# Optimization experiments

Measured on AMD Instinct MI355X. Metric: run time of the kernel, lower is better.

Reference implementation:

```python
import jax, jax.numpy as jnp
import numpy as np

ROUTER_TEMP = 1.0
SCALING = 16.0 / 8.0  # lora_alpha / r


def setup_inputs() -> dict:
    key = jax.random.key(0)
    ks = jax.random.split(key, 6)
    B, S, D, O, E, R = 4, 2048, 4096, 4096, 8, 8
    return {
        "x": jax.random.normal(ks[0], (B, S, D), dtype=jnp.float32),
        "W_base": jax.random.normal(ks[1], (O, D), dtype=jnp.float32) * 0.02,
        "b_base": jax.random.normal(ks[2], (O,), dtype=jnp.float32) * 0.02,
        "lora_A": jax.random.normal(ks[3], (E, R, D), dtype=jnp.float32) * 0.02,
        "lora_B": jax.random.normal(ks[4], (E, O, R), dtype=jnp.float32) * 0.02,
        "router_W": jax.random.normal(ks[5], (E, D), dtype=jnp.float32) * 0.02,
        "router_b": jnp.zeros((E,), dtype=jnp.float32),
    }


def reference(x, W_base, b_base, lora_A, lora_B, router_W, router_b):
    # Base linear: [B,S,D] @ [D,O] + b -> [B,S,O]
    result = jnp.einsum("bsd,od->bso", x, W_base) + b_base

    # Router over mean-pooled sequence: [B,D] -> [B,E]
    x_router = x.mean(axis=1)
    logits = jnp.einsum("bd,ed->be", x_router, router_W) + router_b
    weights = jax.nn.softmax(logits / ROUTER_TEMP, axis=-1)  # [B,E]

    # Per-expert LoRA: down-project to small r, weight by router, up-project.
    h = jnp.einsum("bsd,erd->bser", x, lora_A)            # [B,S,E,r] (small)
    hw = h * weights[:, None, :, None]                      # router-weighted
    lora_out = jnp.einsum("bser,eor->bso", hw, lora_B)     # [B,S,O]

    return result + lora_out * SCALING
```

## Files before the change

kernel.cpp:

```cpp
#include <hip/hip_runtime.h>
#include <hip/hip_bf16.h>


typedef unsigned short u16;
typedef __attribute__((ext_vector_type(8))) short short8;
typedef __attribute__((ext_vector_type(8))) unsigned short u16x8;
typedef __attribute__((ext_vector_type(4))) float f32x4;

#define AS1(p) ((const __attribute__((address_space(1))) void*)(p))
#define AS3(p) ((__attribute__((address_space(3))) void*)(p))

constexpr int KM   = 4224;
constexpr int NOUT = 4096;

__device__ __forceinline__ u16 f2bf(float f) {
    union { float f; unsigned int u; } v; v.f = f;
    unsigned int r = v.u + 0x7fffu + ((v.u >> 16) & 1u);
    return (u16)(r >> 16);
}

__global__ __launch_bounds__(256) void k_convx(const float* __restrict__ x,
                                               u16* __restrict__ Xext,
                                               float* __restrict__ colpart) {
    const int t = threadIdx.x;
    const int row0 = (blockIdx.x >> 7) * 2048 + (blockIdx.x & 127) * 16;
    float4 cs[4] = {{0,0,0,0},{0,0,0,0},{0,0,0,0},{0,0,0,0}};
    for (int r = 0; r < 16; ++r) {
        size_t roff = (size_t)(row0 + r) * 4096;
        #pragma unroll
        for (int g = 0; g < 2; ++g) {
            int col = g * 2048 + t * 8;
            const float4* p = (const float4*)(x + roff + col);
            float4 v0 = p[0], v1 = p[1];
            cs[2*g].x += v0.x; cs[2*g].y += v0.y; cs[2*g].z += v0.z; cs[2*g].w += v0.w;
            cs[2*g+1].x += v1.x; cs[2*g+1].y += v1.y; cs[2*g+1].z += v1.z; cs[2*g+1].w += v1.w;
            u16x8 o;
            o[0]=f2bf(v0.x); o[1]=f2bf(v0.y); o[2]=f2bf(v0.z); o[3]=f2bf(v0.w);
            o[4]=f2bf(v1.x); o[5]=f2bf(v1.y); o[6]=f2bf(v1.z); o[7]=f2bf(v1.w);
            *(u16x8*)(Xext + (size_t)(row0 + r) * KM + col) = o;
        }
    }
    float* cp = colpart + (size_t)blockIdx.x * 4096;
    #pragma unroll
    for (int g = 0; g < 2; ++g) {
        *(float4*)(cp + g * 2048 + t * 8)     = cs[2*g];
        *(float4*)(cp + g * 2048 + t * 8 + 4) = cs[2*g+1];
    }
}

__global__ __launch_bounds__(256) void k_logit(const float* __restrict__ colpart,
                                               const float* __restrict__ rW,
                                               float* __restrict__ logits) {
    const int b = blockIdx.x >> 3, e = blockIdx.x & 7;
    const int t = threadIdx.x;
    const int c0 = t * 16;
    float4 rw[4];
    #pragma unroll
    for (int j = 0; j < 4; ++j) rw[j] = *(const float4*)(rW + e * 4096 + c0 + j * 4);
    float acc = 0.f;
    for (int sc = 0; sc < 128; ++sc) {
        const float4* p = (const float4*)(colpart + ((size_t)(b * 128 + sc)) * 4096 + c0);
        #pragma unroll
        for (int j = 0; j < 4; ++j) {
            float4 v = p[j];
            acc += v.x * rw[j].x + v.y * rw[j].y + v.z * rw[j].z + v.w * rw[j].w;
        }
    }
    __shared__ float red[256];
    red[t] = acc;
    __syncthreads();
    for (int off = 128; off > 0; off >>= 1) {
        if (t < off) red[t] += red[t + off];
        __syncthreads();
    }
    if (t == 0) logits[b * 8 + e] = red[0];
}

__global__ void k_conv8(const float* __restrict__ src, u16* __restrict__ dst) {
    size_t t = (size_t)blockIdx.x * 256 + threadIdx.x;
    size_t base = t * 8;
    size_t row = base >> 12;
    int col = (int)(base & 4095);
    const float4* s = (const float4*)(src + base);
    float4 v0 = s[0], v1 = s[1];
    u16x8 o;
    o[0]=f2bf(v0.x); o[1]=f2bf(v0.y); o[2]=f2bf(v0.z); o[3]=f2bf(v0.w);
    o[4]=f2bf(v1.x); o[5]=f2bf(v1.y); o[6]=f2bf(v1.z); o[7]=f2bf(v1.w);
    *(u16x8*)(dst + row * KM + col) = o;
}

__global__ void k_wlora(const float* __restrict__ lb, u16* __restrict__ Wext) {
    int f = blockIdx.x * 256 + threadIdx.x;
    int e = f >> 15, o = (f >> 3) & 4095, r = f & 7;
    Wext[(size_t)o * KM + 4096 + e * 8 + r] = f2bf(lb[f]);
    Wext[(size_t)(f >> 6) * KM + 4160 + (f & 63)] = 0;
}

__global__ void k_abf(const float* __restrict__ la, u16* __restrict__ Abf) {
    int f = blockIdx.x * 256 + threadIdx.x;
    Abf[f] = f2bf(la[f]);
}

__global__ __launch_bounds__(256) void k_hgemm(const u16* __restrict__ Xb,
                                               const u16* __restrict__ Ab,
                                               const float* __restrict__ logits,
                                               const float* __restrict__ rb,
                                               u16* __restrict__ Hout) {
    __shared__ u16 As[8 * 1024];
    __shared__ u16 Bs[8 * 2048];
    __shared__ float Red[4 * 2048];
    __shared__ float wscL[8];
    const int tid = threadIdx.x, lane = tid & 63, w = tid >> 6;
    const int m0 = blockIdx.x * 32;
    const int b = blockIdx.x >> 6;

    if (tid < 8) {
        float l[8], mx = -1e30f;
        #pragma unroll
        for (int j = 0; j < 8; ++j) {
            l[j] = logits[b * 8 + j] * (1.0f / 2048.0f) + rb[j];
            mx = fmaxf(mx, l[j]);
        }
        float s = 0.f;
        #pragma unroll
        for (int j = 0; j < 8; ++j) s += expf(l[j] - mx);
        wscL[tid] = 2.0f * expf(l[tid] - mx) / s;
    }
    asm volatile("s_waitcnt vmcnt(0)" ::: "memory");

    f32x4 acc[2][4] = {};
    const int kbase = w * 1024;

    auto issue = [&](int it, int buf) {
        const int kt = kbase + it * 32;
        u16* Aw = As + (w * 2 + buf) * 1024;
        u16* Bw = Bs + (w * 2 + buf) * 2048;
        #pragma unroll
        for (int i = 0; i < 2; ++i) {
            int f = lane + i * 64;
            __builtin_amdgcn_global_load_lds(
                AS1(Xb + (size_t)(m0 + (f >> 2)) * KM + kt + (f & 3) * 8),
                AS3(Aw + f * 8), 16, 0, 0);
        }
        #pragma unroll
        for (int i = 0; i < 4; ++i) {
            int f = lane + i * 64;
            __builtin_amdgcn_global_load_lds(
                AS1(Ab + (size_t)(f >> 2) * 4096 + kt + (f & 3) * 8),
                AS3(Bw + f * 8), 16, 0, 0);
        }
    };

    issue(0, 0);
    for (int it = 0; it < 32; ++it) {
        const int buf = it & 1;
        if (it + 1 < 32) {
            issue(it + 1, buf ^ 1);
            asm volatile("s_waitcnt vmcnt(6)" ::: "memory");
        } else {
            asm volatile("s_waitcnt vmcnt(0)" ::: "memory");
        }
        const u16* Aw = As + (w * 2 + buf) * 1024;
        const u16* Bw = Bs + (w * 2 + buf) * 2048;
        short8 af[2], bfr[4];
        #pragma unroll
        for (int mi = 0; mi < 2; ++mi)
            af[mi] = *(const short8*)(Aw + (mi * 16 + (lane & 15)) * 32 + (lane >> 4) * 8);
        #pragma unroll
        for (int nj = 0; nj < 4; ++nj)
            bfr[nj] = *(const short8*)(Bw + (nj * 16 + (lane & 15)) * 32 + (lane >> 4) * 8);
        #pragma unroll
        for (int mi = 0; mi < 2; ++mi)
            #pragma unroll
            for (int nj = 0; nj < 4; ++nj)
                acc[mi][nj] = __builtin_amdgcn_mfma_f32_16x16x32_bf16(af[mi], bfr[nj], acc[mi][nj], 0, 0, 0);
        asm volatile("" ::: "memory");
    }

    const int quad = lane >> 4, lcol = lane & 15;
    #pragma unroll
    for (int mi = 0; mi < 2; ++mi)
        #pragma unroll
        for (int nj = 0; nj < 4; ++nj)
            #pragma unroll
            for (int r = 0; r < 4; ++r)
                Red[w * 2048 + (mi * 16 + quad * 4 + r) * 64 + nj * 16 + lcol] = acc[mi][nj][r];
    __syncthreads();

    const int o = tid * 8, row = o >> 6, col = o & 63;
    float s0=0,s1=0,s2=0,s3=0,s4=0,s5=0,s6=0,s7=0;
    #pragma unroll
    for (int ww = 0; ww < 4; ++ww) {
        const float4* p = (const float4*)(Red + ww * 2048 + o);
        float4 v0 = p[0], v1 = p[1];
        s0+=v0.x; s1+=v0.y; s2+=v0.z; s3+=v0.w;
        s4+=v1.x; s5+=v1.y; s6+=v1.z; s7+=v1.w;
    }
    const float wgt = wscL[col >> 3];
    u16x8 out;
    out[0]=f2bf(s0*wgt); out[1]=f2bf(s1*wgt); out[2]=f2bf(s2*wgt); out[3]=f2bf(s3*wgt);
    out[4]=f2bf(s4*wgt); out[5]=f2bf(s5*wgt); out[6]=f2bf(s6*wgt); out[7]=f2bf(s7*wgt);
    *(u16x8*)(Hout + (size_t)(m0 + row) * KM + 4096 + col) = out;
    u16x8 zz = {0,0,0,0,0,0,0,0};
    *(u16x8*)(Hout + (size_t)(m0 + (tid >> 3)) * KM + 4160 + (tid & 7) * 8) = zz;
}


#define LDB_(bufB) do { \
    const char* bp_ = ldsc + bBaseB + (bufB); \
    _Pragma("unroll") \
    for (int nj_ = 0; nj_ < 4; ++nj_) { \
        bf[nj_][0] = *(const short8*)(bp_ + nj_ * 2048 + rdk0); \
        bf[nj_][1] = *(const short8*)(bp_ + nj_ * 2048 + rdk1); \
    } \
} while (0)

#define LDA_(bufB, pq) do { \
    const char* ap_ = ldsc + aBaseB + (bufB) + (pq) * 4096; \
    af[0][0] = *(const short8*)(ap_ + rdk0); \
    af[0][1] = *(const short8*)(ap_ + rdk1); \
    af[1][0] = *(const short8*)(ap_ + 2048 + rdk0); \
    af[1][1] = *(const short8*)(ap_ + 2048 + rdk1); \
} while (0)

#define MFMA_(pq) do { \
    __builtin_amdgcn_s_barrier(); \
    asm volatile("s_waitcnt lgkmcnt(0)" ::: "memory"); \
    __builtin_amdgcn_sched_barrier(0); \
    __builtin_amdgcn_s_setprio(1); \
    _Pragma("unroll") \
    for (int q_ = 0; q_ < 2; ++q_) { \
        _Pragma("unroll") \
        for (int nj_ = 0; nj_ < 4; ++nj_) { \
            acc[(pq)*2+q_][nj_] = __builtin_amdgcn_mfma_f32_16x16x32_bf16(af[q_][0], bf[nj_][0], acc[(pq)*2+q_][nj_], 0, 0, 0); \
            acc[(pq)*2+q_][nj_] = __builtin_amdgcn_mfma_f32_16x16x32_bf16(af[q_][1], bf[nj_][1], acc[(pq)*2+q_][nj_], 0, 0, 0); \
        } \
    } \
    __builtin_amdgcn_s_setprio(0); \
    __builtin_amdgcn_sched_barrier(0); \
} while (0)

#define ENDPH_() __builtin_amdgcn_s_barrier()

__global__ __launch_bounds__(512, 2) void k_main(const u16* __restrict__ A, const u16* __restrict__ B,
                                                 const float* __restrict__ bias, float* __restrict__ C) {
    __shared__ __align__(16) u16 lds[65536];
    const char* ldsc = (const char*)lds;
    const int tid = threadIdx.x;
    const int lane = tid & 63;
    const int w = tid >> 6;
    const int wm = w >> 2;
    const int wn = w & 3;
    const int lr = lane & 15, hi = lane >> 4;

    const int bid = blockIdx.x;
    const int swz = (bid & 7) * 64 + (bid >> 3);
    const int m0 = (swz >> 4) * 256;
    const int n0 = (swz & 15) * 256;

    const int csw = (lr & 7) << 4;
    const int rdk0 = lr * 128 + ((hi * 16) ^ csw);
    const int rdk1 = lr * 128 + ((64 + hi * 16) ^ csw);
    const int aBaseB = wm * 16384;
    const int bBaseB = 32768 + (wn >> 1) * 16384 + (wn & 1) * 8192;

    const int srow = tid >> 3;
    const int scol = ((tid & 7) ^ ((tid >> 3) & 7)) * 8;
    const int so0 = srow * KM + scol;
    const int so1 = (64 + srow) * KM + scol;
    const u16* Am0 = A + (size_t)m0 * KM;
    const u16* Am1 = A + (size_t)(m0 + 128) * KM;
    const u16* Bm0 = B + (size_t)n0 * KM;
    const u16* Bm1 = B + (size_t)(n0 + 128) * KM;
    u16* ldst = lds + tid * 8;

    auto stage = [&](const u16* src, int t, int regionEl) {
        __builtin_amdgcn_global_load_lds(AS1(src + so0 + t * 64), AS3(ldst + regionEl), 16, 0, 0);
        __builtin_amdgcn_global_load_lds(AS1(src + so1 + t * 64), AS3(ldst + regionEl + 4096), 16, 0, 0);
    };

    f32x4 acc[8][4] = {};

    stage(Bm0, 0, 16384);
    stage(Bm1, 0, 24576);
    stage(Am0, 0, 0);
    stage(Am1, 0, 8192);
    stage(Bm0, 1, 32768 + 16384);
    stage(Bm1, 1, 32768 + 24576);
    asm volatile("s_waitcnt vmcnt(4)" ::: "memory");
    __builtin_amdgcn_s_barrier();

    #pragma unroll 1
    for (int i = 0; i < 33; ++i) {
        const int t = i * 2;
        const bool nl = (i < 32);
        short8 af[2][2];
        short8 bf[4][2];
        LDB_(0); LDA_(0, 0);
        stage(Am0, t + 1, 32768);
        MFMA_(0); ENDPH_();
        LDA_(0, 1);
        stage(Am1, t + 1, 32768 + 8192);
        MFMA_(1); ENDPH_();
        LDA_(0, 2);
        if (nl) stage(Bm0, t + 2, 16384);
        MFMA_(2); ENDPH_();
        LDA_(0, 3);
        if (nl) stage(Bm1, t + 2, 24576);
        MFMA_(3);
        if (nl) { asm volatile("s_waitcnt vmcnt(4)" ::: "memory"); }
        else    { asm volatile("s_waitcnt vmcnt(0)" ::: "memory"); }
        ENDPH_();
        LDB_(65536); LDA_(65536, 0);
        if (nl) stage(Am0, t + 2, 0);
        MFMA_(0); ENDPH_();
        LDA_(65536, 1);
        if (nl) stage(Am1, t + 2, 8192);
        MFMA_(1); ENDPH_();
        LDA_(65536, 2);
        if (nl) stage(Bm0, t + 3, 32768 + 16384);
        MFMA_(2); ENDPH_();
        LDA_(65536, 3);
        if (nl) stage(Bm1, t + 3, 32768 + 24576);
        MFMA_(3);
        if (nl) { asm volatile("s_waitcnt vmcnt(4)" ::: "memory"); }
        ENDPH_();
    }

    const int colb = n0 + wn * 64 + lr;
    const int rowb = m0 + wm * 128 + hi * 4;
    #pragma unroll
    for (int nj = 0; nj < 4; ++nj) {
        const int col = colb + nj * 16;
        const float bv = bias[col];
        #pragma unroll
        for (int mi = 0; mi < 8; ++mi) {
            float* Cp = C + (size_t)(rowb + mi * 16) * NOUT + col;
            #pragma unroll
            for (int r = 0; r < 4; ++r)
                Cp[(size_t)r * NOUT] = acc[mi][nj][r] + bv;
        }
    }
}

extern "C" void kernel_launch(void* const* d_in, const int* in_sizes, int n_in,
                              void* d_out, int out_size, void* d_ws, size_t ws_size,
                              hipStream_t stream) {
    const float* x  = (const float*)d_in[0];
    const float* Wb = (const float*)d_in[1];
    const float* bb = (const float*)d_in[2];
    const float* lA = (const float*)d_in[3];
    const float* lB = (const float*)d_in[4];
    const float* rW = (const float*)d_in[5];
    const float* rb = (const float*)d_in[6];
    float* out = (float*)d_out;

    char* ws = (char*)d_ws;
    float* logits = (float*)ws;
    u16* Abf      = (u16*)(ws + 256);
    u16* Xext     = (u16*)(ws + 524800);
    u16* Wext     = (u16*)(ws + 524800 + 69206016ULL);
    float* colpart = (float*)Wext;

    k_abf   <<<1024, 256, 0, stream>>>(lA, Abf);
    k_convx <<<512,  256, 0, stream>>>(x, Xext, colpart);
    k_logit <<<32,   256, 0, stream>>>(colpart, rW, logits);
    k_hgemm <<<256,  256, 0, stream>>>(Xext, Abf, logits, rb, Xext);
    k_conv8 <<<8192, 256, 0, stream>>>(Wb, Wext);
    k_wlora <<<1024, 256, 0, stream>>>(lB, Wext);
    k_main  <<<512,  512, 0, stream>>>(Xext, Wext, bb, out);
}
```

Before: 564.1 us.

## Split router reduction into column-sum and logit kernels; refine GEMM A-load waits

The router logit kernel is split in two. A 64-block kernel now sums the per-chunk column partials, and a tiny kernel takes the dot product with the router weights, replacing a 32-block kernel that streamed all partials. In the main GEMM, A-tile staging is split into two halves with finer vmcnt waits, so the first half can be consumed before the second finishes. The MFMA loop order is also reordered k-outer so both k-halves are not serialized on the same accumulator. This adds an extra launch and a colsum buffer in the workspace, and the tighter wait counts must match the issued loads exactly.

```diff
diff --git a/kernel.cpp b/kernel.cpp
--- a/kernel.cpp
+++ b/kernel.cpp
@@ -48,23 +48,29 @@
     }
 }
 
-__global__ __launch_bounds__(256) void k_logit(const float* __restrict__ colpart,
-                                               const float* __restrict__ rW,
-                                               float* __restrict__ logits) {
+__global__ __launch_bounds__(256) void k_red(const float* __restrict__ colpart,
+                                             float* __restrict__ colsum) {
+    const int b = blockIdx.x >> 4;
+    const int col = (blockIdx.x & 15) * 256 + threadIdx.x;
+    const float* p = colpart + (size_t)b * 128 * 4096 + col;
+    float acc = 0.f;
+    #pragma unroll 4
+    for (int sc = 0; sc < 128; ++sc) acc += p[(size_t)sc * 4096];
+    colsum[b * 4096 + col] = acc;
+}
+
+__global__ __launch_bounds__(256) void k_lgt(const float* __restrict__ colsum,
+                                             const float* __restrict__ rW,
+                                             float* __restrict__ logits) {
     const int b = blockIdx.x >> 3, e = blockIdx.x & 7;
     const int t = threadIdx.x;
-    const int c0 = t * 16;
-    float4 rw[4];
-    #pragma unroll
-    for (int j = 0; j < 4; ++j) rw[j] = *(const float4*)(rW + e * 4096 + c0 + j * 4);
+    const float4* cp = (const float4*)(colsum + b * 4096 + t * 16);
+    const float4* wp = (const float4*)(rW + e * 4096 + t * 16);
     float acc = 0.f;
-    for (int sc = 0; sc < 128; ++sc) {
-        const float4* p = (const float4*)(colpart + ((size_t)(b * 128 + sc)) * 4096 + c0);
-        #pragma unroll
-        for (int j = 0; j < 4; ++j) {
-            float4 v = p[j];
-            acc += v.x * rw[j].x + v.y * rw[j].y + v.z * rw[j].z + v.w * rw[j].w;
-        }
+    #pragma unroll
+    for (int j = 0; j < 4; ++j) {
+        float4 c = cp[j], w = wp[j];
+        acc += c.x * w.x + c.y * w.y + c.z * w.z + c.w * w.w;
     }
     __shared__ float red[256];
     red[t] = acc;
@@ -229,18 +235,18 @@
     __builtin_amdgcn_sched_barrier(0); \
     __builtin_amdgcn_s_setprio(1); \
     _Pragma("unroll") \
-    for (int q_ = 0; q_ < 2; ++q_) { \
+    for (int k_ = 0; k_ < 2; ++k_) \
         _Pragma("unroll") \
-        for (int nj_ = 0; nj_ < 4; ++nj_) { \
-            acc[(pq)*2+q_][nj_] = __builtin_amdgcn_mfma_f32_16x16x32_bf16(af[q_][0], bf[nj_][0], acc[(pq)*2+q_][nj_], 0, 0, 0); \
-            acc[(pq)*2+q_][nj_] = __builtin_amdgcn_mfma_f32_16x16x32_bf16(af[q_][1], bf[nj_][1], acc[(pq)*2+q_][nj_], 0, 0, 0); \
-        } \
-    } \
+        for (int q_ = 0; q_ < 2; ++q_) \
+            _Pragma("unroll") \
+            for (int nj_ = 0; nj_ < 4; ++nj_) \
+                acc[(pq)*2+q_][nj_] = __builtin_amdgcn_mfma_f32_16x16x32_bf16(af[q_][k_], bf[nj_][k_], acc[(pq)*2+q_][nj_], 0, 0, 0); \
     __builtin_amdgcn_s_setprio(0); \
     __builtin_amdgcn_sched_barrier(0); \
 } while (0)
 
 #define ENDPH_() __builtin_amdgcn_s_barrier()
+#define VM_(n)   asm volatile("s_waitcnt vmcnt(" #n ")" ::: "memory")
 
 __global__ __launch_bounds__(512, 2) void k_main(const u16* __restrict__ A, const u16* __restrict__ B,
                                                  const float* __restrict__ bias, float* __restrict__ C) {
@@ -274,20 +280,27 @@
     const u16* Bm1 = B + (size_t)(n0 + 128) * KM;
     u16* ldst = lds + tid * 8;
 
-    auto stage = [&](const u16* src, int t, int regionEl) {
+    auto stageB = [&](const u16* src, int t, int regionEl) {
         __builtin_amdgcn_global_load_lds(AS1(src + so0 + t * 64), AS3(ldst + regionEl), 16, 0, 0);
         __builtin_amdgcn_global_load_lds(AS1(src + so1 + t * 64), AS3(ldst + regionEl + 4096), 16, 0, 0);
     };
+    auto stageA = [&](int t, int bufEl, int which) {
+        const size_t ro = (size_t)(which * 64) * KM;
+        __builtin_amdgcn_global_load_lds(AS1(Am0 + ro + so0 + t * 64),
+                                         AS3(ldst + bufEl + which * 4096), 16, 0, 0);
+        __builtin_amdgcn_global_load_lds(AS1(Am1 + ro + so0 + t * 64),
+                                         AS3(ldst + bufEl + 8192 + which * 4096), 16, 0, 0);
+    };
 
     f32x4 acc[8][4] = {};
 
-    stage(Bm0, 0, 16384);
-    stage(Bm1, 0, 24576);
-    stage(Am0, 0, 0);
-    stage(Am1, 0, 8192);
-    stage(Bm0, 1, 32768 + 16384);
-    stage(Bm1, 1, 32768 + 24576);
-    asm volatile("s_waitcnt vmcnt(4)" ::: "memory");
+    stageB(Bm0, 0, 16384);
+    stageB(Bm1, 0, 24576);
+    stageA(0, 0, 0);
+    stageA(0, 0, 1);
+    stageB(Bm0, 1, 32768 + 16384);
+    stageB(Bm1, 1, 32768 + 24576);
+    VM_(6);
     __builtin_amdgcn_s_barrier();
 
     #pragma unroll 1
@@ -297,33 +310,34 @@
         short8 af[2][2];
         short8 bf[4][2];
         LDB_(0); LDA_(0, 0);
-        stage(Am0, t + 1, 32768);
+        stageA(t + 1, 32768, 0);
         MFMA_(0); ENDPH_();
         LDA_(0, 1);
-        stage(Am1, t + 1, 32768 + 8192);
-        MFMA_(1); ENDPH_();
+        stageA(t + 1, 32768, 1);
+        MFMA_(1); VM_(8); ENDPH_();
         LDA_(0, 2);
-        if (nl) stage(Bm0, t + 2, 16384);
+        if (nl) stageB(Bm0, t + 2, 16384);
         MFMA_(2); ENDPH_();
         LDA_(0, 3);
-        if (nl) stage(Bm1, t + 2, 24576);
+        if (nl) stageB(Bm1, t + 2, 24576);
         MFMA_(3);
-        if (nl) { asm volatile("s_waitcnt vmcnt(4)" ::: "memory"); }
-        else    { asm volatile("s_waitcnt vmcnt(0)" ::: "memory"); }
+        if (nl) { VM_(6); } else { VM_(2); }
         ENDPH_();
         LDB_(65536); LDA_(65536, 0);
-        if (nl) stage(Am0, t + 2, 0);
+        if (nl) stageA(t + 2, 0, 0);
         MFMA_(0); ENDPH_();
         LDA_(65536, 1);
-        if (nl) stage(Am1, t + 2, 8192);
-        MFMA_(1); ENDPH_();
+        if (nl) stageA(t + 2, 0, 1);
+        MFMA_(1);
+        if (nl) { VM_(8); } else { VM_(0); }
+        ENDPH_();
         LDA_(65536, 2);
-        if (nl) stage(Bm0, t + 3, 32768 + 16384);
+        if (nl) stageB(Bm0, t + 3, 32768 + 16384);
         MFMA_(2); ENDPH_();
         LDA_(65536, 3);
-        if (nl) stage(Bm1, t + 3, 32768 + 24576);
+        if (nl) stageB(Bm1, t + 3, 32768 + 24576);
         MFMA_(3);
-        if (nl) { asm volatile("s_waitcnt vmcnt(4)" ::: "memory"); }
+        if (nl) { VM_(6); }
         ENDPH_();
     }
 
@@ -361,10 +375,12 @@
     u16* Xext     = (u16*)(ws + 524800);
     u16* Wext     = (u16*)(ws + 524800 + 69206016ULL);
     float* colpart = (float*)Wext;
+    float* colsum  = (float*)((char*)Wext + (16u << 20));
 
     k_abf   <<<1024, 256, 0, stream>>>(lA, Abf);
     k_convx <<<512,  256, 0, stream>>>(x, Xext, colpart);
-    k_logit <<<32,   256, 0, stream>>>(colpart, rW, logits);
+    k_red   <<<64,   256, 0, stream>>>(colpart, colsum);
+    k_lgt   <<<32,   256, 0, stream>>>(colsum, rW, logits);
     k_hgemm <<<256,  256, 0, stream>>>(Xext, Abf, logits, rb, Xext);
     k_conv8 <<<8192, 256, 0, stream>>>(Wb, Wext);
     k_wlora <<<1024, 256, 0, stream>>>(lB, Wext);
```

New measurement: 552.0 us. 2.2% less time.
